# Optimization experiments

Hardware: AMD Instinct MI355X
Metric: run time of the kernel (lower is better)

The kernel has to match this reference:

```python
import jax, jax.numpy as jnp
import numpy as np

C = 10      # output (digit) capsules
L = 16      # output capsule dim
ROUTING = 3
EPS = 1e-7  # keras backend epsilon


def squash(s):
    # n^2/(1+n^2)/(n+eps) * s, norm over last axis
    n = jnp.linalg.norm(s, axis=-1, keepdims=True)
    return (n ** 2) / (1.0 + n ** 2) / (n + EPS) * s


def setup_inputs() -> dict:
    key = jax.random.key(0)
    k1, k2 = jax.random.split(key)
    B, H, W_, iC, iL = 128, 12, 12, 32, 8
    N = H * W_ * iC  # 4608
    inputs = jax.random.normal(k1, (B, H, W_, iC, iL), dtype=jnp.float32)
    W = jax.random.normal(k2, (N, iL, L * C), dtype=jnp.float32) * 0.05
    biases = jnp.zeros((C, L), dtype=jnp.float32)
    return {"inputs": inputs, "W": W, "biases": biases}


def reference(inputs, W, biases):
    B = inputs.shape[0]
    N = W.shape[0]
    x = inputs.reshape(B, N, -1)                      # [B, N, input_L]
    u = jnp.einsum('bnj,njk->bnk', x, W)              # [B, N, C*L]
    u = u.reshape(B, N, C, L)
    b = jnp.zeros((B, N, C, 1), dtype=u.dtype)
    v = None
    for r in range(ROUTING):
        c = jax.nn.softmax(b, axis=2)                 # over output capsules
        s = jnp.sum(u * c, axis=1, keepdims=True)     # [B, 1, C, L]
        s = s + biases
        v = squash(s)
        if r < ROUTING - 1:
            b = b + jnp.sum(u * v, axis=-1, keepdims=True)
    return v[:, 0]                                    # [B, C, L]
```

## Files before the change

kernel.cpp:

```cpp
#include <hip/hip_runtime.h>
#include <math.h>


namespace {
constexpr int B_   = 128;
constexpr int N_   = 4608;
constexpr int C_   = 10;
constexpr int L_   = 16;
constexpr int CL   = C_ * L_;
constexpr int NCHK = 256;
constexpr int TILE_N = N_ / NCHK;
constexpr int BCL  = B_ * CL;
constexpr int RED_G = 16;
constexpr int RED_K = NCHK / RED_G;
constexpr int WBLK = (N_ * CL) / 256;
constexpr int XBLK = (B_ * N_) / 256;
}

typedef _Float16 v4h __attribute__((ext_vector_type(4)));
typedef _Float16 v8h __attribute__((ext_vector_type(8)));
typedef float    v4f __attribute__((ext_vector_type(4)));

__global__ __launch_bounds__(256)
void conv_pack(const float* __restrict__ W, const float* __restrict__ x,
               v8h* __restrict__ Wt, v8h* __restrict__ xh)
{
  if ((int)blockIdx.x < WBLK) {
    const int t  = blockIdx.x * 256 + threadIdx.x;
    const int n  = t / CL, cl = t % CL;
    const float* p = W + (size_t)n * (8 * CL) + cl;
    v8h o;
#pragma unroll
    for (int j = 0; j < 8; ++j) o[j] = (_Float16)p[j * CL];
    Wt[t] = o;
  } else {
    const int t = ((int)blockIdx.x - WBLK) * 256 + threadIdx.x;
    const float4 a = ((const float4*)x)[(size_t)t * 2 + 0];
    const float4 b = ((const float4*)x)[(size_t)t * 2 + 1];
    v8h o = { (_Float16)a.x, (_Float16)a.y, (_Float16)a.z, (_Float16)a.w,
              (_Float16)b.x, (_Float16)b.y, (_Float16)b.z, (_Float16)b.w };
    xh[t] = o;
  }
}

template<int MODE>
__global__ __launch_bounds__(256, 2)
void pass_kernel(const _Float16* __restrict__ xh,
                 const _Float16* __restrict__ Wt,
                 const float* __restrict__ va,
                 const float* __restrict__ vb,
                 float* __restrict__ partials)
{
  const int lane = threadIdx.x & 63;
  const int wid  = threadIdx.x >> 6;
  const int bl   = lane & 15;
  const int hi   = lane >> 4;
  const int b    = blockIdx.y * 64 + wid * 16 + bl;
  const int n0   = blockIdx.x * TILE_N;
  const bool lo  = lane < 32;
  const int kh   = (lane >> 4) & 1;

  v4f vv[C_];
  if (MODE >= 1) {
#pragma unroll
    for (int c = 0; c < C_; ++c) {
      vv[c] = *(const v4f*)(va + ((size_t)b * C_ + c) * L_ + hi * 4);
      if (MODE == 2)
        vv[c] += *(const v4f*)(vb + ((size_t)b * C_ + c) * L_ + hi * 4);
    }
  }

  const v4f zf = {0.f, 0.f, 0.f, 0.f};
  v4f sacc[C_];
#pragma unroll
  for (int c = 0; c < C_; ++c) sacc[c] = zf;

  const _Float16* xp = xh + ((size_t)b * N_ + n0) * 8 + kh * 4;
  const _Float16* wp = Wt + ((size_t)n0 * CL + bl) * 8 + kh * 4;

  v4h xf = {};
  v4h wf[C_];
#pragma unroll
  for (int c = 0; c < C_; ++c) wf[c] = xf;

  for (int nn = 0; nn < TILE_N; ++nn) {
    if (lo) {
      xf = *(const v4h*)(xp + nn * 8);
#pragma unroll
      for (int c = 0; c < C_; ++c)
        wf[c] = *(const v4h*)(wp + (size_t)nn * (CL * 8) + c * (16 * 8));
    }

    if (MODE == 0) {
#pragma unroll
      for (int c = 0; c < C_; ++c)
        sacc[c] = __builtin_amdgcn_mfma_f32_16x16x16f16(wf[c], xf, sacc[c], 0, 0, 0);
    } else {
      v4f u[C_];
#pragma unroll
      for (int c = 0; c < C_; ++c)
        u[c] = __builtin_amdgcn_mfma_f32_16x16x16f16(wf[c], xf, zf, 0, 0, 0);

      float tt[C_];
#pragma unroll
      for (int c = 0; c < C_; ++c) {
        float t = u[c][0] * vv[c][0];
        t = fmaf(u[c][1], vv[c][1], t);
        t = fmaf(u[c][2], vv[c][2], t);
        t = fmaf(u[c][3], vv[c][3], t);
        tt[c] = t;
      }
#pragma unroll
      for (int c = 0; c < C_; ++c) {
        tt[c] += __shfl_xor(tt[c], 16);
        tt[c] += __shfl_xor(tt[c], 32);
      }
      float es = 0.f;
#pragma unroll
      for (int c = 0; c < C_; ++c) { tt[c] = __expf(tt[c]); es += tt[c]; }
      const float rs = __builtin_amdgcn_rcpf(es);
#pragma unroll
      for (int c = 0; c < C_; ++c) {
        const float w = tt[c] * rs;
#pragma unroll
        for (int i = 0; i < 4; ++i)
          sacc[c][i] = fmaf(w, u[c][i], sacc[c][i]);
      }
    }
  }

  float* pout = partials + ((size_t)blockIdx.x * B_ + b) * CL + hi * 4;
#pragma unroll
  for (int c = 0; c < C_; ++c)
    *(v4f*)(pout + c * L_) = sacc[c];
}

__global__ __launch_bounds__(256)
void reduce_a(const float* __restrict__ p, float* __restrict__ p2) {
  const int t   = blockIdx.x * 256 + threadIdx.x;
  const int idx = t % BCL;
  const int g   = t / BCL;
  float a = 0.f;
#pragma unroll
  for (int k = 0; k < RED_K; ++k)
    a += p[(size_t)(g * RED_K + k) * BCL + idx];
  p2[t] = a;
}

__global__ __launch_bounds__(256)
void reduce_b(const float* __restrict__ p2, const float* __restrict__ biases,
              float* __restrict__ vout, float scale) {
  const int idx = blockIdx.x * 256 + threadIdx.x;
  float a = 0.f;
#pragma unroll
  for (int g = 0; g < RED_G; ++g) a += p2[(size_t)g * BCL + idx];
  const float s = a * scale + biases[idx % CL];
  float n2 = s * s;
#pragma unroll
  for (int o = 8; o; o >>= 1) n2 += __shfl_xor(n2, o, 16);
  const float n = sqrtf(n2);
  const float f = n2 / ((1.f + n2) * (n + 1e-7f));
  vout[idx] = f * s;
}

extern "C" void kernel_launch(void* const* d_in, const int* in_sizes, int n_in,
                              void* d_out, int out_size, void* d_ws, size_t ws_size,
                              hipStream_t stream) {
  const float* x      = (const float*)d_in[0];
  const float* W      = (const float*)d_in[1];
  const float* biases = (const float*)d_in[2];
  float* out = (float*)d_out;

  _Float16* Wt  = (_Float16*)d_ws;
  _Float16* xhp = Wt + (size_t)N_ * CL * 8;
  float* partials = (float*)(xhp + (size_t)B_ * N_ * 8);
  float* p2 = partials + (size_t)NCHK * BCL;
  float* v0 = p2 + (size_t)RED_G * BCL;
  float* v1 = v0 + BCL;

  conv_pack<<<WBLK + XBLK, 256, 0, stream>>>(W, x, (v8h*)Wt, (v8h*)xhp);

  const dim3 pg(NCHK, 2), pb(256);

  pass_kernel<0><<<pg, pb, 0, stream>>>(xhp, Wt, nullptr, nullptr, partials);
  reduce_a<<<(RED_G * BCL) / 256, 256, 0, stream>>>(partials, p2);
  reduce_b<<<BCL / 256, 256, 0, stream>>>(p2, biases, v0, 0.1f);

  pass_kernel<1><<<pg, pb, 0, stream>>>(xhp, Wt, v0, nullptr, partials);
  reduce_a<<<(RED_G * BCL) / 256, 256, 0, stream>>>(partials, p2);
  reduce_b<<<BCL / 256, 256, 0, stream>>>(p2, biases, v1, 1.0f);

  pass_kernel<2><<<pg, pb, 0, stream>>>(xhp, Wt, v0, v1, partials);
  reduce_a<<<(RED_G * BCL) / 256, 256, 0, stream>>>(partials, p2);
  reduce_b<<<BCL / 256, 256, 0, stream>>>(p2, biases, out, 1.0f);
}
```

Baseline: 169.6 us.

## Pack two capsules per MFMA in first pass, use fdot2 agreement, more chunks

```diff
diff --git a/kernel.cpp b/kernel.cpp
--- a/kernel.cpp
+++ b/kernel.cpp
@@ -8,7 +8,7 @@
 constexpr int C_   = 10;
 constexpr int L_   = 16;
 constexpr int CL   = C_ * L_;
-constexpr int NCHK = 256;
+constexpr int NCHK = 576;
 constexpr int TILE_N = N_ / NCHK;
 constexpr int BCL  = B_ * CL;
 constexpr int RED_G = 16;
@@ -17,9 +17,28 @@
 constexpr int XBLK = (B_ * N_) / 256;
 }
 
+typedef _Float16 h2  __attribute__((ext_vector_type(2)));
 typedef _Float16 v4h __attribute__((ext_vector_type(4)));
 typedef _Float16 v8h __attribute__((ext_vector_type(8)));
 typedef float    v4f __attribute__((ext_vector_type(4)));
+
+__device__ inline h2 pkrtz(float a, float b) {
+  return __builtin_bit_cast(h2, __builtin_amdgcn_cvt_pkrtz(a, b));
+}
+
+#if defined(__has_builtin)
+#if __has_builtin(__builtin_amdgcn_fdot2)
+#define HAVE_FDOT2 1
+#endif
+#endif
+
+__device__ inline float fdot2(h2 a, h2 b, float c) {
+#ifdef HAVE_FDOT2
+  return __builtin_amdgcn_fdot2(a, b, c, false);
+#else
+  return c + (float)a[0] * (float)b[0] + (float)a[1] * (float)b[1];
+#endif
+}
 
 __global__ __launch_bounds__(256)
 void conv_pack(const float* __restrict__ W, const float* __restrict__ x,
@@ -44,7 +63,7 @@
 }
 
 template<int MODE>
-__global__ __launch_bounds__(256, 2)
+__global__ __launch_bounds__(256, 3)
 void pass_kernel(const _Float16* __restrict__ xh,
                  const _Float16* __restrict__ Wt,
                  const float* __restrict__ va,
@@ -57,16 +76,19 @@
   const int hi   = lane >> 4;
   const int b    = blockIdx.y * 64 + wid * 16 + bl;
   const int n0   = blockIdx.x * TILE_N;
+  const int joff = (hi & 1) * 4;
+  const int noff = (MODE == 0) ? (hi >> 1) : 0;
   const bool lo  = lane < 32;
-  const int kh   = (lane >> 4) & 1;
-
-  v4f vv[C_];
+
+  h2 vvh[C_][2];
   if (MODE >= 1) {
 #pragma unroll
     for (int c = 0; c < C_; ++c) {
-      vv[c] = *(const v4f*)(va + ((size_t)b * C_ + c) * L_ + hi * 4);
+      v4f t = *(const v4f*)(va + ((size_t)b * C_ + c) * L_ + hi * 4);
       if (MODE == 2)
-        vv[c] += *(const v4f*)(vb + ((size_t)b * C_ + c) * L_ + hi * 4);
+        t += *(const v4f*)(vb + ((size_t)b * C_ + c) * L_ + hi * 4);
+      vvh[c][0] = pkrtz(t[0], t[1]);
+      vvh[c][1] = pkrtz(t[2], t[3]);
     }
   }
 
@@ -75,21 +97,19 @@
 #pragma unroll
   for (int c = 0; c < C_; ++c) sacc[c] = zf;
 
-  const _Float16* xp = xh + ((size_t)b * N_ + n0) * 8 + kh * 4;
-  const _Float16* wp = Wt + ((size_t)n0 * CL + bl) * 8 + kh * 4;
-
-  v4h xf = {};
-  v4h wf[C_];
-#pragma unroll
-  for (int c = 0; c < C_; ++c) wf[c] = xf;
-
-  for (int nn = 0; nn < TILE_N; ++nn) {
-    if (lo) {
-      xf = *(const v4h*)(xp + nn * 8);
-#pragma unroll
-      for (int c = 0; c < C_; ++c)
-        wf[c] = *(const v4h*)(wp + (size_t)nn * (CL * 8) + c * (16 * 8));
+  const _Float16* xp = xh + ((size_t)b * N_ + n0 + noff) * 8 + joff;
+  const _Float16* wp = Wt + ((size_t)(n0 + noff) * CL + bl) * 8 + joff;
+
+  constexpr int NSTEP = (MODE == 0) ? 2 : 1;
+  for (int nn = 0; nn < TILE_N; nn += NSTEP) {
+    v4h xf = *(const v4h*)(xp + nn * 8);
+    if (MODE >= 1) {
+      if (!lo) { v4h z = {}; xf = z; }
     }
+    v4h wf[C_];
+#pragma unroll
+    for (int c = 0; c < C_; ++c)
+      wf[c] = *(const v4h*)(wp + (size_t)nn * (CL * 8) + c * (16 * 8));
 
     if (MODE == 0) {
 #pragma unroll
@@ -104,11 +124,10 @@
       float tt[C_];
 #pragma unroll
       for (int c = 0; c < C_; ++c) {
-        float t = u[c][0] * vv[c][0];
-        t = fmaf(u[c][1], vv[c][1], t);
-        t = fmaf(u[c][2], vv[c][2], t);
-        t = fmaf(u[c][3], vv[c][3], t);
-        tt[c] = t;
+        const h2 ua = pkrtz(u[c][0], u[c][1]);
+        const h2 ub = pkrtz(u[c][2], u[c][3]);
+        float t = fdot2(ua, vvh[c][0], 0.f);
+        tt[c] = fdot2(ub, vvh[c][1], t);
       }
 #pragma unroll
       for (int c = 0; c < C_; ++c) {
@@ -172,8 +191,8 @@
   float* out = (float*)d_out;
 
   _Float16* Wt  = (_Float16*)d_ws;
-  _Float16* xhp = Wt + (size_t)N_ * CL * 8;
-  float* partials = (float*)(xhp + (size_t)B_ * N_ * 8);
+  _Float16* xhp = Wt + (size_t)N_ * CL * 8 + 64;
+  float* partials = (float*)(xhp + (size_t)B_ * N_ * 8 + 64);
   float* p2 = partials + (size_t)NCHK * BCL;
   float* v0 = p2 + (size_t)RED_G * BCL;
   float* v1 = v0 + BCL;
```

Measured after the change: 410.0 us. 142% more time.
